# Kernel tuning notes

Measured on AMD Instinct MI355X. Metric: run time of the kernel, lower is better.

Reference implementation:

```python
import jax, jax.numpy as jnp
import numpy as np

B, F, D, A = 1024, 33, 128, 128  # batch, num_fields, embed_dim, attn_size (A must equal gnn dim)

def setup_inputs() -> dict:
    key = jax.random.key(0)
    k1, k2, k3, k4 = jax.random.split(key, 4)
    gnn_feature = jax.random.normal(k1, (B, A), dtype=jnp.float32)
    x = jax.random.normal(k2, (B, F, D), dtype=jnp.float32)
    # attention Linear(embed_dim -> attn_size): weight (A, D), bias (A,)
    lim = 1.0 / np.sqrt(D)
    attn_W = jax.random.uniform(k3, (A, D), minval=-lim, maxval=lim, dtype=jnp.float32)
    attn_b = jax.random.uniform(k4, (A,), minval=-lim, maxval=lim, dtype=jnp.float32)
    return {"gnn_feature": gnn_feature, "x": x, "attn_W": attn_W, "attn_b": attn_b}

def reference(gnn_feature, x, attn_W, attn_b):
    num_fields = x.shape[1]
    row, col = np.triu_indices(num_fields, k=1)  # P = F*(F-1)/2 pairs
    inner = x[:, row] * x[:, col]                # [B, P, D]
    fm = jax.nn.relu(jnp.einsum('bpd,ad->bpa', inner, attn_W) + attn_b)  # [B, P, A]
    # bmm(gnn[b,1,A], fm[b,p,A,1]) -> dot product per pair, softmax over pairs
    scores = jnp.einsum('ba,bpa->bp', gnn_feature, fm)  # [B, P]
    attn = jax.nn.softmax(scores, axis=1)               # [B, P]
    attn_output = jnp.einsum('bp,bpd->bd', attn, inner) * 100.0  # [B, D]
    return jnp.concatenate([gnn_feature, attn_output], axis=1)   # [B, A+D]
```

## Files before the change

kernel.cpp:

```cpp
#include <hip/hip_runtime.h>

#define FN 33
#define DN 128
#define AN 128
#define PN 528
#define MTN 33
#define XS 136
#define TS 36

typedef __attribute__((ext_vector_type(8))) _Float16 half8;
typedef __attribute__((ext_vector_type(4))) float f32x4;
typedef __attribute__((ext_vector_type(4))) unsigned int u32x4;

__device__ __forceinline__ unsigned int pkrtz(float a, float b) {
  return __builtin_bit_cast(unsigned int, __builtin_amdgcn_cvt_pkrtz(a, b));
}

__device__ __forceinline__ float row_sum16(float v) {
  v += __builtin_bit_cast(float, __builtin_amdgcn_update_dpp(0, __builtin_bit_cast(int, v), 0x128, 0xF, 0xF, false));
  v += __builtin_bit_cast(float, __builtin_amdgcn_update_dpp(0, __builtin_bit_cast(int, v), 0x124, 0xF, 0xF, false));
  v += __builtin_bit_cast(float, __builtin_amdgcn_update_dpp(0, __builtin_bit_cast(int, v), 0x122, 0xF, 0xF, false));
  v += __builtin_bit_cast(float, __builtin_amdgcn_update_dpp(0, __builtin_bit_cast(int, v), 0x121, 0xF, 0xF, false));
  return v;
}

__global__ __launch_bounds__(256, 2)
void afm_kernel(const float* __restrict__ gnn, const float* __restrict__ xg,
                const float* __restrict__ Wg,  const float* __restrict__ bg,
                float* __restrict__ out)
{
  __shared__ __align__(16) _Float16 Wl[2048 * 8];
  __shared__ __align__(16) _Float16 xh[FN * XS];
  __shared__ __align__(16) float attn2d[FN * TS];
  __shared__ __align__(16) float scores_s[PN];
  __shared__ __align__(16) float part[256];
  __shared__ unsigned short rowcol[PN];
  __shared__ float red[8];

  const int tid  = threadIdx.x;
  const int b    = blockIdx.x;
  const int wave = tid >> 6;
  const int lane = tid & 63;
  const int q    = lane >> 4;
  const int u    = lane & 15;

  for (int idx = tid; idx < FN * TS; idx += 256) attn2d[idx] = 0.0f;

  const f32x4* xg4 = (const f32x4*)(xg + (size_t)b * FN * DN);
  for (int idx = tid; idx < (FN * DN) / 4; idx += 256) {
    f32x4 v = xg4[idx];
    int i  = idx >> 5;
    int d0 = (idx & 31) << 2;
    *(uint2*)&xh[i * XS + d0] = make_uint2(pkrtz(v.x, v.y), pkrtz(v.z, v.w));
  }
  #pragma unroll
  for (int s = 0; s < 8; s++) {
    int C  = tid + s * 256;
    int n  = C >> 8;
    int kk = (C >> 6) & 3;
    int qq = (C >> 4) & 3;
    int uu = C & 15;
    const float* src = Wg + (size_t)(n * 16 + uu) * DN + kk * 32 + qq * 8;
    f32x4 w0 = *(const f32x4*)(src);
    f32x4 w1 = *(const f32x4*)(src + 4);
    u32x4 pk;
    pk.x = pkrtz(w0.x, w0.y);
    pk.y = pkrtz(w0.z, w0.w);
    pk.z = pkrtz(w1.x, w1.y);
    pk.w = pkrtz(w1.z, w1.w);
    *(u32x4*)&Wl[C * 8] = pk;
  }
  for (int p = tid; p < PN; p += 256) {
    int i = 0, rem = p;
    while (rem >= FN - 1 - i) { rem -= FN - 1 - i; i++; }
    rowcol[p] = (unsigned short)(i | ((i + 1 + rem) << 8));
  }
  __syncthreads();

  half8 Bf[8][4];
  #pragma unroll
  for (int n = 0; n < 8; n++)
    #pragma unroll
    for (int kk = 0; kk < 4; kk++) {
      Bf[n][kk] = *(const half8*)&Wl[((n * 4 + kk) * 64 + lane) * 8];
      asm volatile("" : "+v"(Bf[n][kk]));
    }
  float garr[8], barr[8];
  #pragma unroll
  for (int n = 0; n < 8; n++) {
    garr[n] = gnn[(size_t)b * AN + n * 16 + u];
    barr[n] = bg[n * 16 + u];
    asm volatile("" : "+v"(garr[n]), "+v"(barr[n]));
  }

  for (int mt = wave; mt < MTN; mt += 4) {
    const int p = mt * 16 + u;
    const unsigned int rc = rowcol[p];
    const int r = rc & 255, c = rc >> 8;

    half8 Af[4];
    #pragma unroll
    for (int kk = 0; kk < 4; kk++) {
      half8 xr = *(const half8*)&xh[r * XS + kk * 32 + q * 8];
      half8 xc = *(const half8*)&xh[c * XS + kk * 32 + q * 8];
      Af[kk] = xr * xc;
    }

    f32x4 acc[8];
    #pragma unroll
    for (int n = 0; n < 8; n++) acc[n] = (f32x4){0.f, 0.f, 0.f, 0.f};
    #pragma unroll
    for (int kk = 0; kk < 4; kk++)
      #pragma unroll
      for (int n = 0; n < 8; n++)
        acc[n] = __builtin_amdgcn_mfma_f32_16x16x32_f16(Af[kk], Bf[n][kk], acc[n], 0, 0, 0);

    float sc[4] = {0.f, 0.f, 0.f, 0.f};
    #pragma unroll
    for (int n = 0; n < 8; n++)
      #pragma unroll
      for (int rr = 0; rr < 4; rr++) {
        float fmv = fmaxf(acc[n][rr] + barr[n], 0.f);
        sc[rr] = fmaf(fmv, garr[n], sc[rr]);
      }
    #pragma unroll
    for (int rr = 0; rr < 4; rr++) sc[rr] = row_sum16(sc[rr]);
    if (u == 0)
      *(f32x4*)&scores_s[mt * 16 + q * 4] = (f32x4){sc[0], sc[1], sc[2], sc[3]};
  }
  __syncthreads();

  float s0 = scores_s[tid];
  float s1 = scores_s[tid + 256];
  float s2 = (tid < 16) ? scores_s[tid + 512] : -3.4e38f;
  float m = fmaxf(fmaxf(s0, s1), s2);
  #pragma unroll
  for (int off = 32; off >= 1; off >>= 1) m = fmaxf(m, __shfl_xor(m, off, 64));
  if (lane == 0) red[wave] = m;
  __syncthreads();
  const float smax = fmaxf(fmaxf(red[0], red[1]), fmaxf(red[2], red[3]));

  float e0 = __expf(s0 - smax);
  float e1 = __expf(s1 - smax);
  float e2 = (tid < 16) ? __expf(s2 - smax) : 0.f;
  {
    unsigned int rc = rowcol[tid];
    attn2d[(rc & 255) * TS + ((rc >> 8) - (rc & 255) - 1)] = e0;
    rc = rowcol[tid + 256];
    attn2d[(rc & 255) * TS + ((rc >> 8) - (rc & 255) - 1)] = e1;
    if (tid < 16) {
      rc = rowcol[tid + 512];
      attn2d[(rc & 255) * TS + ((rc >> 8) - (rc & 255) - 1)] = e2;
    }
  }
  float lsum = e0 + e1 + e2;
  #pragma unroll
  for (int off = 32; off >= 1; off >>= 1) lsum += __shfl_xor(lsum, off, 64);
  if (lane == 0) red[4 + wave] = lsum;
  __syncthreads();
  const float Z = red[4] + red[5] + red[6] + red[7];

  {
    const int d = tid & 127;
    const int h = tid >> 7;
    float xcol[36];
    #pragma unroll
    for (int i = 0; i < FN; i++) xcol[i] = (float)xh[i * XS + d];
    xcol[33] = 0.f; xcol[34] = 0.f; xcol[35] = 0.f;

    float acc = 0.f;
    const int ibeg = h * 16, iend = ibeg + 16;
    #pragma unroll
    for (int i = 0; i < 32; i++) {
      if (i < ibeg || i >= iend) continue;
      const int L = FN - 1 - i;
      const int nf4 = (L + 3) >> 2;
      float ti = 0.f;
      #pragma unroll
      for (int t = 0; t < 8; t++) {
        if (t >= nf4) break;
        f32x4 a4 = *(const f32x4*)&attn2d[i * TS + t * 4];
        ti = fmaf(a4.x, xcol[i + 1 + t * 4 + 0], ti);
        ti = fmaf(a4.y, xcol[i + 1 + t * 4 + 1], ti);
        ti = fmaf(a4.z, xcol[i + 1 + t * 4 + 2], ti);
        ti = fmaf(a4.w, xcol[i + 1 + t * 4 + 3], ti);
      }
      acc = fmaf(xcol[i], ti, acc);
    }
    part[tid] = acc;
  }
  __syncthreads();
  if (tid < DN) {
    float tot = part[tid] + part[tid + 128];
    out[(size_t)b * (AN + DN) + AN + tid] = tot * (100.0f / Z);
  } else {
    const int a = tid - 128;
    out[(size_t)b * (AN + DN) + a] = gnn[(size_t)b * AN + a];
  }
}

extern "C" void kernel_launch(void* const* d_in, const int* in_sizes, int n_in,
                              void* d_out, int out_size, void* d_ws, size_t ws_size,
                              hipStream_t stream) {
  (void)n_in; (void)out_size; (void)d_ws; (void)ws_size;
  const float* gnn  = (const float*)d_in[0];
  const float* x    = (const float*)d_in[1];
  const float* W    = (const float*)d_in[2];
  const float* bias = (const float*)d_in[3];
  float* out = (float*)d_out;
  const int Bn = in_sizes[0] / AN;
  afm_kernel<<<dim3(Bn), dim3(256), 0, stream>>>(gnn, x, W, bias, out);
}
```

Measured before the change: 107.6 us.

## Split attention columns across wave pairs, drop LDS weight staging, raise occupancy

```diff
diff --git a/kernel.cpp b/kernel.cpp
--- a/kernel.cpp
+++ b/kernel.cpp
@@ -4,7 +4,6 @@
 #define DN 128
 #define AN 128
 #define PN 528
-#define MTN 33
 #define XS 136
 #define TS 36
 
@@ -24,15 +23,14 @@
   return v;
 }
 
-__global__ __launch_bounds__(256, 2)
+__global__ __launch_bounds__(256, 4)
 void afm_kernel(const float* __restrict__ gnn, const float* __restrict__ xg,
                 const float* __restrict__ Wg,  const float* __restrict__ bg,
                 float* __restrict__ out)
 {
-  __shared__ __align__(16) _Float16 Wl[2048 * 8];
   __shared__ __align__(16) _Float16 xh[FN * XS];
   __shared__ __align__(16) float attn2d[FN * TS];
-  __shared__ __align__(16) float scores_s[PN];
+  __shared__ __align__(16) float sp[2][PN];
   __shared__ __align__(16) float part[256];
   __shared__ unsigned short rowcol[PN];
   __shared__ float red[8];
@@ -43,6 +41,31 @@
   const int lane = tid & 63;
   const int q    = lane >> 4;
   const int u    = lane & 15;
+  const int nh   = wave & 1;
+  const int mh   = wave >> 1;
+
+  half8 Bf[4][4];
+  float garr[4], barr[4];
+  #pragma unroll
+  for (int nn = 0; nn < 4; nn++) {
+    const int a = (nh * 4 + nn) * 16 + u;
+    const float* src = Wg + (size_t)a * DN + q * 8;
+    #pragma unroll
+    for (int kk = 0; kk < 4; kk++) {
+      f32x4 w0 = *(const f32x4*)(src + kk * 32);
+      f32x4 w1 = *(const f32x4*)(src + kk * 32 + 4);
+      u32x4 pk;
+      pk.x = pkrtz(w0.x, w0.y);
+      pk.y = pkrtz(w0.z, w0.w);
+      pk.z = pkrtz(w1.x, w1.y);
+      pk.w = pkrtz(w1.z, w1.w);
+      Bf[nn][kk] = __builtin_bit_cast(half8, pk);
+      asm volatile("" : "+v"(Bf[nn][kk]));
+    }
+    garr[nn] = gnn[(size_t)b * AN + a];
+    barr[nn] = bg[a];
+    asm volatile("" : "+v"(garr[nn]), "+v"(barr[nn]));
+  }
 
   for (int idx = tid; idx < FN * TS; idx += 256) attn2d[idx] = 0.0f;
 
@@ -53,23 +76,6 @@
     int d0 = (idx & 31) << 2;
     *(uint2*)&xh[i * XS + d0] = make_uint2(pkrtz(v.x, v.y), pkrtz(v.z, v.w));
   }
-  #pragma unroll
-  for (int s = 0; s < 8; s++) {
-    int C  = tid + s * 256;
-    int n  = C >> 8;
-    int kk = (C >> 6) & 3;
-    int qq = (C >> 4) & 3;
-    int uu = C & 15;
-    const float* src = Wg + (size_t)(n * 16 + uu) * DN + kk * 32 + qq * 8;
-    f32x4 w0 = *(const f32x4*)(src);
-    f32x4 w1 = *(const f32x4*)(src + 4);
-    u32x4 pk;
-    pk.x = pkrtz(w0.x, w0.y);
-    pk.y = pkrtz(w0.z, w0.w);
-    pk.z = pkrtz(w1.x, w1.y);
-    pk.w = pkrtz(w1.z, w1.w);
-    *(u32x4*)&Wl[C * 8] = pk;
-  }
   for (int p = tid; p < PN; p += 256) {
     int i = 0, rem = p;
     while (rem >= FN - 1 - i) { rem -= FN - 1 - i; i++; }
@@ -77,62 +83,48 @@
   }
   __syncthreads();
 
-  half8 Bf[8][4];
-  #pragma unroll
-  for (int n = 0; n < 8; n++)
+  const int mt_beg = mh ? 17 : 0;
+  const int mt_end = mh ? 33 : 17;
+  unsigned int rc_next = rowcol[mt_beg * 16 + u];
+  for (int mt = mt_beg; mt < mt_end; ++mt) {
+    const unsigned int rc = rc_next;
+    if (mt + 1 < mt_end) rc_next = rowcol[(mt + 1) * 16 + u];
+    const int r = rc & 255, c = rc >> 8;
+    const _Float16* xr_base = &xh[r * XS + q * 8];
+    const _Float16* xc_base = &xh[c * XS + q * 8];
+
+    f32x4 acc[4];
+    #pragma unroll
+    for (int nn = 0; nn < 4; nn++) acc[nn] = (f32x4){0.f, 0.f, 0.f, 0.f};
+
     #pragma unroll
     for (int kk = 0; kk < 4; kk++) {
-      Bf[n][kk] = *(const half8*)&Wl[((n * 4 + kk) * 64 + lane) * 8];
-      asm volatile("" : "+v"(Bf[n][kk]));
-    }
-  float garr[8], barr[8];
-  #pragma unroll
-  for (int n = 0; n < 8; n++) {
-    garr[n] = gnn[(size_t)b * AN + n * 16 + u];
-    barr[n] = bg[n * 16 + u];
-    asm volatile("" : "+v"(garr[n]), "+v"(barr[n]));
-  }
-
-  for (int mt = wave; mt < MTN; mt += 4) {
-    const int p = mt * 16 + u;
-    const unsigned int rc = rowcol[p];
-    const int r = rc & 255, c = rc >> 8;
-
-    half8 Af[4];
-    #pragma unroll
-    for (int kk = 0; kk < 4; kk++) {
-      half8 xr = *(const half8*)&xh[r * XS + kk * 32 + q * 8];
-      half8 xc = *(const half8*)&xh[c * XS + kk * 32 + q * 8];
-      Af[kk] = xr * xc;
-    }
-
-    f32x4 acc[8];
-    #pragma unroll
-    for (int n = 0; n < 8; n++) acc[n] = (f32x4){0.f, 0.f, 0.f, 0.f};
-    #pragma unroll
-    for (int kk = 0; kk < 4; kk++)
+      half8 xr = *(const half8*)(xr_base + kk * 32);
+      half8 xc = *(const half8*)(xc_base + kk * 32);
+      half8 af = xr * xc;
       #pragma unroll
-      for (int n = 0; n < 8; n++)
-        acc[n] = __builtin_amdgcn_mfma_f32_16x16x32_f16(Af[kk], Bf[n][kk], acc[n], 0, 0, 0);
+      for (int nn = 0; nn < 4; nn++)
+        acc[nn] = __builtin_amdgcn_mfma_f32_16x16x32_f16(af, Bf[nn][kk], acc[nn], 0, 0, 0);
+    }
 
     float sc[4] = {0.f, 0.f, 0.f, 0.f};
     #pragma unroll
-    for (int n = 0; n < 8; n++)
+    for (int nn = 0; nn < 4; nn++)
       #pragma unroll
       for (int rr = 0; rr < 4; rr++) {
-        float fmv = fmaxf(acc[n][rr] + barr[n], 0.f);
-        sc[rr] = fmaf(fmv, garr[n], sc[rr]);
+        float fmv = fmaxf(acc[nn][rr] + barr[nn], 0.f);
+        sc[rr] = fmaf(fmv, garr[nn], sc[rr]);
       }
     #pragma unroll
     for (int rr = 0; rr < 4; rr++) sc[rr] = row_sum16(sc[rr]);
     if (u == 0)
-      *(f32x4*)&scores_s[mt * 16 + q * 4] = (f32x4){sc[0], sc[1], sc[2], sc[3]};
-  }
-  __syncthreads();
-
-  float s0 = scores_s[tid];
-  float s1 = scores_s[tid + 256];
-  float s2 = (tid < 16) ? scores_s[tid + 512] : -3.4e38f;
+      *(f32x4*)&sp[nh][mt * 16 + q * 4] = (f32x4){sc[0], sc[1], sc[2], sc[3]};
+  }
+  __syncthreads();
+
+  float s0 = sp[0][tid] + sp[1][tid];
+  float s1 = sp[0][tid + 256] + sp[1][tid + 256];
+  float s2 = (tid < 16) ? (sp[0][tid + 512] + sp[1][tid + 512]) : -3.4e38f;
   float m = fmaxf(fmaxf(s0, s1), s2);
   #pragma unroll
   for (int off = 32; off >= 1; off >>= 1) m = fmaxf(m, __shfl_xor(m, off, 64));
@@ -169,16 +161,14 @@
     xcol[33] = 0.f; xcol[34] = 0.f; xcol[35] = 0.f;
 
     float acc = 0.f;
-    const int ibeg = h * 16, iend = ibeg + 16;
     #pragma unroll
     for (int i = 0; i < 32; i++) {
-      if (i < ibeg || i >= iend) continue;
+      if ((i & 1) != h) continue;
       const int L = FN - 1 - i;
       const int nf4 = (L + 3) >> 2;
       float ti = 0.f;
       #pragma unroll
-      for (int t = 0; t < 8; t++) {
-        if (t >= nf4) break;
+      for (int t = 0; t < nf4; t++) {
         f32x4 a4 = *(const f32x4*)&attn2d[i * TS + t * 4];
         ti = fmaf(a4.x, xcol[i + 1 + t * 4 + 0], ti);
         ti = fmaf(a4.y, xcol[i + 1 + t * 4 + 1], ti);
```

Result: slower. 112.6 us (+4.7%).
